# Performance work log

Measured on AMD Instinct MI355X. Metric: run time of the kernel, lower is better.

Reference implementation:

```python
import jax, jax.numpy as jnp
import numpy as np

B, S, D, H = 2, 2048, 1024, 16
DK = D // H
MAX_REL = 2047          # clip range for relative distances
REL_DIM = 64            # rel_embedding dim, summed over


def setup_inputs() -> dict:
    key = jax.random.key(0)
    ks = jax.random.split(key, 12)
    sc = 1.0 / np.sqrt(D)
    inp = {
        "q": jax.random.normal(ks[0], (B, S, D), jnp.float32),
        "k": jax.random.normal(ks[1], (B, S, D), jnp.float32),
        "v": jax.random.normal(ks[2], (B, S, D), jnp.float32),
        "Wq": jax.random.normal(ks[3], (D, D), jnp.float32) * sc,
        "bq": jnp.zeros((D,), jnp.float32),
        "Wk": jax.random.normal(ks[4], (D, D), jnp.float32) * sc,
        "bk": jnp.zeros((D,), jnp.float32),
        "Wv": jax.random.normal(ks[5], (D, D), jnp.float32) * sc,
        "bv": jnp.zeros((D,), jnp.float32),
        "Wo": jax.random.normal(ks[6], (D, D), jnp.float32) * sc,
        "bo": jnp.zeros((D,), jnp.float32),
        "rel_table": jax.random.normal(ks[7], (2 * MAX_REL + 1, REL_DIM), jnp.float32) * 0.02,
        "mask": jnp.tril(jnp.ones((1, 1, S, S), jnp.bool_)),  # causal
    }
    return inp


def reference(q, k, v, Wq, bq, Wk, bk, Wv, bv, Wo, bo, rel_table, mask):
    def split_heads(x):
        # [B,S,D] -> [B,H,S,DK]
        return x.reshape(B, -1, H, DK).transpose(0, 2, 1, 3)

    Q = split_heads(q @ Wq + bq)
    K = split_heads(k @ Wk + bk)
    V = split_heads(v @ Wv + bv)

    scores = jnp.einsum("bhqd,bhkd->bhqk", Q, K) / jnp.sqrt(jnp.float32(DK))

    # relative position bias: table[clip(j - i)] summed over rel dim -> [S,S]
    rel_idx = jnp.clip(jnp.arange(S)[None, :] - jnp.arange(S)[:, None],
                       -MAX_REL, MAX_REL) + MAX_REL
    rel_bias = rel_table[rel_idx].sum(-1)  # [S,S]
    scores = scores + rel_bias[None, None]

    scores = jnp.where(mask, scores, jnp.float32(-1e20))
    attn = jax.nn.softmax(scores, axis=-1)

    out = jnp.einsum("bhqk,bhkd->bhqd", attn, V)
    out = out.transpose(0, 2, 1, 3).reshape(B, -1, D)
    return out @ Wo + bo
```

## Files before the change

### kernel.cpp

```cpp
#include <hip/hip_runtime.h>

#define SEQ 2048
#define DIM 1024
#define NH 16
#define HD 64
#define NB 2

typedef __bf16 bf16x8 __attribute__((ext_vector_type(8)));
typedef float f32x4 __attribute__((ext_vector_type(4)));
typedef float f32x4v __attribute__((ext_vector_type(4)));
typedef float f32x4u __attribute__((ext_vector_type(4), aligned(4)));
typedef unsigned short us8 __attribute__((ext_vector_type(8)));
typedef unsigned short us4 __attribute__((ext_vector_type(4)));

#define LOG2E 1.44269504f

__device__ __forceinline__ unsigned short bfbits(float f) {
  __bf16 h = (__bf16)f;
  return __builtin_bit_cast(unsigned short, h);
}

__global__ __launch_bounds__(256) void wconv4_kernel(
    const float* __restrict__ W0, const float* __restrict__ W1,
    const float* __restrict__ W2, const float* __restrict__ W3,
    unsigned short* __restrict__ Wt, const float* __restrict__ rel_table,
    float* __restrict__ relsum) {
  int z = blockIdx.z;
  int tid = threadIdx.x;
  if (z == 4) {
    int ti = blockIdx.y * 16 + blockIdx.x;
    int i = ti * 256 + tid;
    if (i < 4095) {
      const f32x4v* row = reinterpret_cast<const f32x4v*>(rel_table + (size_t)i * 64);
      float s = 0.f;
      for (int d = 0; d < 16; ++d) {
        f32x4v v = row[d];
        s += v[0] + v[1] + v[2] + v[3];
      }
      relsum[i] = s * LOG2E;
    }
    return;
  }
  __shared__ unsigned short T[64][68];
  const float* W = (z == 0) ? W0 : (z == 1) ? W1 : (z == 2) ? W2 : W3;
  unsigned short* out = Wt + (size_t)z * 1024 * 1024;
  int r0 = blockIdx.y * 64;
  int c0 = blockIdx.x * 64;
  for (int it = 0; it < 4; ++it) {
    int s = tid + it * 256;
    int r = s >> 4;
    int c4 = (s & 15) * 4;
    f32x4v v = *reinterpret_cast<const f32x4v*>(W + (size_t)(r0 + r) * 1024 + c0 + c4);
    us4 o;
    o[0] = bfbits(v[0]); o[1] = bfbits(v[1]); o[2] = bfbits(v[2]); o[3] = bfbits(v[3]);
    *reinterpret_cast<us4*>(&T[r][c4]) = o;
  }
  __syncthreads();
  for (int it = 0; it < 2; ++it) {
    int s = tid + it * 256;
    int n = s >> 3;
    int k8 = (s & 7) * 8;
    us8 o;
    for (int e = 0; e < 8; ++e) o[e] = T[k8 + e][n];
    *reinterpret_cast<us8*>(out + (size_t)(c0 + n) * 1024 + r0 + k8) = o;
  }
}

__global__ __launch_bounds__(256) void gemm_qkv_kernel(
    const float* __restrict__ Aq, const float* __restrict__ Ak,
    const float* __restrict__ Av, const unsigned short* __restrict__ WTb,
    const float* __restrict__ bq, const float* __restrict__ bk,
    const float* __restrict__ bv, unsigned short* __restrict__ Qb,
    unsigned short* __restrict__ Kb, unsigned short* __restrict__ Vt,
    float qscale) {
  constexpr int N = 1024, K = 1024;
  int o = (blockIdx.x & 7) * 192 + (blockIdx.x >> 3);
  int row0 = (o / 48) * 128;
  int colz = o % 48;
  int z = colz >> 4;
  int col0 = (colz & 15) * 64;
  const float* A = (z == 0) ? Aq : (z == 1) ? Ak : Av;
  const unsigned short* WT = WTb + (size_t)z * N * K;
  const float* bias = (z == 0) ? bq : (z == 1) ? bk : bv;
  float oscale = (z == 0) ? qscale : 1.0f;

  int tid = threadIdx.x;
  int w = tid >> 6;
  int lane = tid & 63;
  int lg = lane >> 4;
  int li = lane & 15;
  int wr = (w >> 1) * 64;
  int wc = (w & 1) * 32;

  __shared__ unsigned short As[2][128][72];
  __shared__ unsigned short Ws[2][64][72];

  f32x4v af32[8];
  us8 wreg[2];

#define GLOAD(KS)                                                         \
  {                                                                       \
    int k0 = (KS) * 64;                                                   \
    for (int it = 0; it < 8; ++it) {                                      \
      int s = tid + it * 256;                                             \
      int r = s >> 4;                                                     \
      int cg = (s & 15) * 4;                                              \
      af32[it] = *reinterpret_cast<const f32x4v*>(                        \
          A + (size_t)(row0 + r) * K + k0 + cg);                          \
    }                                                                     \
    for (int it = 0; it < 2; ++it) {                                      \
      int s = tid + it * 256;                                             \
      int c = s >> 3;                                                     \
      int kg = (s & 7) * 8;                                               \
      wreg[it] = *reinterpret_cast<const us8*>(                           \
          WT + (size_t)(col0 + c) * K + k0 + kg);                         \
    }                                                                     \
  }

#define SWRITE(B)                                                         \
  {                                                                       \
    for (int it = 0; it < 8; ++it) {                                      \
      int s = tid + it * 256;                                             \
      int r = s >> 4;                                                     \
      int cg = (s & 15) * 4;                                              \
      us4 o2;                                                             \
      o2[0] = bfbits(af32[it][0]); o2[1] = bfbits(af32[it][1]);           \
      o2[2] = bfbits(af32[it][2]); o2[3] = bfbits(af32[it][3]);           \
      *reinterpret_cast<us4*>(&As[B][r][cg]) = o2;                        \
    }                                                                     \
    for (int it = 0; it < 2; ++it) {                                      \
      int s = tid + it * 256;                                             \
      int c = s >> 3;                                                     \
      int kg = (s & 7) * 8;                                               \
      *reinterpret_cast<us8*>(&Ws[B][c][kg]) = wreg[it];                  \
    }                                                                     \
  }

  f32x4 acc[4][2] = {};

  GLOAD(0);
  SWRITE(0);
  GLOAD(1);
  __syncthreads();

  for (int ks = 0; ks < 16; ++ks) {
    if (ks < 15) SWRITE((ks + 1) & 1);
    if (ks < 14) GLOAD(ks + 2);
    int B = ks & 1;
    for (int kk = 0; kk < 2; ++kk) {
      bf16x8 af[4], bfr[2];
      for (int m = 0; m < 4; ++m)
        af[m] = *reinterpret_cast<const bf16x8*>(&As[B][wr + m * 16 + li][kk * 32 + lg * 8]);
      for (int n = 0; n < 2; ++n)
        bfr[n] = *reinterpret_cast<const bf16x8*>(&Ws[B][wc + n * 16 + li][kk * 32 + lg * 8]);
      for (int m = 0; m < 4; ++m)
        for (int n = 0; n < 2; ++n)
          acc[m][n] = __builtin_amdgcn_mfma_f32_16x16x32_bf16(af[m], bfr[n], acc[m][n], 0, 0, 0);
    }
    __syncthreads();
  }

  for (int m = 0; m < 4; ++m)
    for (int n = 0; n < 2; ++n) {
      int row = row0 + wr + m * 16 + lg * 4;
      int col = col0 + wc + n * 16 + li;
      float v4[4];
      for (int r = 0; r < 4; ++r) v4[r] = (acc[m][n][r] + bias[col]) * oscale;
      if (z == 2) {
        int bb = row >> 11, seq = row & 2047;
        int hh = col >> 6, dk = col & 63;
        us4 o4;
        o4[0] = bfbits(v4[0]); o4[1] = bfbits(v4[1]);
        o4[2] = bfbits(v4[2]); o4[3] = bfbits(v4[3]);
        *reinterpret_cast<us4*>(
            Vt + ((size_t)(bb * NH + hh) * HD + dk) * SEQ + seq) = o4;
      } else {
        unsigned short* Cp = (z == 0) ? Qb : Kb;
        for (int r = 0; r < 4; ++r)
          Cp[(size_t)(row + r) * N + col] = bfbits(v4[r]);
      }
    }
#undef GLOAD
#undef SWRITE
}

__global__ __launch_bounds__(256) void gemm_out_kernel(
    const unsigned short* __restrict__ A, const unsigned short* __restrict__ WT,
    const float* __restrict__ bias, float* __restrict__ Cp) {
  constexpr int N = 1024, K = 1024;
  int o = ((blockIdx.x & 7) << 6) | (blockIdx.x >> 3);
  int col0 = (o & 15) * 64;
  int row0 = (o >> 4) * 128;
  int tid = threadIdx.x;
  int w = tid >> 6;
  int lane = tid & 63;
  int lg = lane >> 4;
  int li = lane & 15;
  int wr = (w >> 1) * 64;
  int wc = (w & 1) * 32;

  __shared__ unsigned short As[2][128][72];
  __shared__ unsigned short Ws[2][64][72];

  us8 ab16[4];
  us8 wreg[2];

#define GLOAD(KS)                                                         \
  {                                                                       \
    int k0 = (KS) * 64;                                                   \
    for (int it = 0; it < 4; ++it) {                                      \
      int s = tid + it * 256;                                             \
      int r = s >> 3;                                                     \
      int cg = (s & 7) * 8;                                               \
      ab16[it] = *reinterpret_cast<const us8*>(                           \
          A + (size_t)(row0 + r) * K + k0 + cg);                          \
    }                                                                     \
    for (int it = 0; it < 2; ++it) {                                      \
      int s = tid + it * 256;                                             \
      int c = s >> 3;                                                     \
      int kg = (s & 7) * 8;                                               \
      wreg[it] = *reinterpret_cast<const us8*>(                           \
          WT + (size_t)(col0 + c) * K + k0 + kg);                         \
    }                                                                     \
  }

#define SWRITE(B)                                                         \
  {                                                                       \
    for (int it = 0; it < 4; ++it) {                                      \
      int s = tid + it * 256;                                             \
      int r = s >> 3;                                                     \
      int cg = (s & 7) * 8;                                               \
      *reinterpret_cast<us8*>(&As[B][r][cg]) = ab16[it];                  \
    }                                                                     \
    for (int it = 0; it < 2; ++it) {                                      \
      int s = tid + it * 256;                                             \
      int c = s >> 3;                                                     \
      int kg = (s & 7) * 8;                                               \
      *reinterpret_cast<us8*>(&Ws[B][c][kg]) = wreg[it];                  \
    }                                                                     \
  }

  f32x4 acc[4][2] = {};

  GLOAD(0);
  SWRITE(0);
  GLOAD(1);
  __syncthreads();

  for (int ks = 0; ks < 16; ++ks) {
    if (ks < 15) SWRITE((ks + 1) & 1);
    if (ks < 14) GLOAD(ks + 2);
    int B = ks & 1;
    for (int kk = 0; kk < 2; ++kk) {
      bf16x8 af[4], bfr[2];
      for (int m = 0; m < 4; ++m)
        af[m] = *reinterpret_cast<const bf16x8*>(&As[B][wr + m * 16 + li][kk * 32 + lg * 8]);
      for (int n = 0; n < 2; ++n)
        bfr[n] = *reinterpret_cast<const bf16x8*>(&Ws[B][wc + n * 16 + li][kk * 32 + lg * 8]);
      for (int m = 0; m < 4; ++m)
        for (int n = 0; n < 2; ++n)
          acc[m][n] = __builtin_amdgcn_mfma_f32_16x16x32_bf16(af[m], bfr[n], acc[m][n], 0, 0, 0);
    }
    __syncthreads();
  }

  for (int m = 0; m < 4; ++m)
    for (int n = 0; n < 2; ++n)
      for (int r = 0; r < 4; ++r) {
        int row = row0 + wr + m * 16 + lg * 4 + r;
        int col = col0 + wc + n * 16 + li;
        Cp[(size_t)row * N + col] = acc[m][n][r] + bias[col];
      }
#undef GLOAD
#undef SWRITE
}

__global__ __launch_bounds__(256) void attn_kernel(
    const unsigned short* __restrict__ Qb, const unsigned short* __restrict__ Kb,
    const unsigned short* __restrict__ Vt, const float* __restrict__ relsum,
    unsigned short* __restrict__ Ob) {
  int o = ((blockIdx.x & 7) << 6) | (blockIdx.x >> 3);
  int p = o & 15;
  int h = (o >> 4) & 15;
  int b = o >> 8;

  int tid = threadIdx.x;
  int w = tid >> 6;
  int lane = tid & 63;
  int lg = lane >> 4;
  int li = lane & 15;

  __shared__ unsigned short Ks[128][72];
  __shared__ unsigned short VtF[2][64 * 72];
  __shared__ __bf16 Ps[4][16][136];
  __shared__ float rel_lds[2176];

  for (int it = 0; it < 3; ++it) {
    int slot = tid + it * 256;
    if (slot < 544)
      *reinterpret_cast<f32x4v*>(&rel_lds[slot * 4]) =
          *reinterpret_cast<const f32x4v*>(&relsum[slot * 4]);
  }

  int key0 = tid >> 3;
  int cg0 = (tid & 7) * 8;
  int dk0 = tid >> 3;
  int k8 = (tid & 7) * 8;
  const unsigned short* kptr = Kb + ((size_t)(b * SEQ + key0)) * DIM + h * HD + cg0;
  const unsigned short* vtp = Vt + ((size_t)(b * NH + h) * HD + dk0) * SEQ + k8;

  unsigned vidx0 = ((unsigned)(dk0 * 72 + k8)) ^ ((((unsigned)dk0 >> 3) & 7u) << 3);
  unsigned vidx1 = ((unsigned)((dk0 + 32) * 72 + k8)) ^
                   ((((unsigned)(dk0 + 32) >> 3) & 7u) << 3);

  us8 krg[4], vrg[4];

#define LOAD_REGS(TT)                                                     \
  {                                                                       \
    size_t koff = (size_t)(TT) * 128 * DIM;                               \
    krg[0] = *reinterpret_cast<const us8*>(kptr + koff);                  \
    krg[1] = *reinterpret_cast<const us8*>(kptr + koff + 32 * DIM);       \
    krg[2] = *reinterpret_cast<const us8*>(kptr + koff + 64 * DIM);       \
    krg[3] = *reinterpret_cast<const us8*>(kptr + koff + 96 * DIM);       \
    vrg[0] = *reinterpret_cast<const us8*>(vtp + (TT) * 128);             \
    vrg[1] = *reinterpret_cast<const us8*>(vtp + 32 * SEQ + (TT) * 128);  \
    vrg[2] = *reinterpret_cast<const us8*>(vtp + (TT) * 128 + 64);        \
    vrg[3] = *reinterpret_cast<const us8*>(vtp + 32 * SEQ + (TT) * 128 + 64); \
  }

#define WRITE_TILE()                                                     \
  {                                                                      \
    *reinterpret_cast<us8*>(&Ks[key0][cg0]) = krg[0];                    \
    *reinterpret_cast<us8*>(&Ks[key0 + 32][cg0]) = krg[1];               \
    *reinterpret_cast<us8*>(&Ks[key0 + 64][cg0]) = krg[2];               \
    *reinterpret_cast<us8*>(&Ks[key0 + 96][cg0]) = krg[3];               \
    *reinterpret_cast<us8*>(&VtF[0][vidx0]) = vrg[0];                    \
    *reinterpret_cast<us8*>(&VtF[0][vidx1]) = vrg[1];                    \
    *reinterpret_cast<us8*>(&VtF[1][vidx0]) = vrg[2];                    \
    *reinterpret_cast<us8*>(&VtF[1][vidx1]) = vrg[3];                    \
  }

  LOAD_REGS(0);

  for (int ph = 0; ph < 2; ++ph) {
    int qt = ph ? p : (31 - p);
    int nkv = (qt + 2) >> 1;

    int qrow = qt * 64 + w * 16 + li;
    const unsigned short* qb = Qb + ((size_t)(b * SEQ + qrow)) * DIM + h * HD;
    bf16x8 qa0 = *reinterpret_cast<const bf16x8*>(qb + lg * 8);
    bf16x8 qa1 = *reinterpret_cast<const bf16x8*>(qb + 32 + lg * 8);

    f32x4 o_acc[4] = {};
    float m_row[4], l_row[4];
    for (int r = 0; r < 4; ++r) { m_row[r] = -3e38f; l_row[r] = 0.f; }
    int i0 = qt * 64 + w * 16 + lg * 4;

    for (int t = 0; t < nkv; ++t) {
      __syncthreads();
      WRITE_TILE();
      __syncthreads();

      if (!(ph == 1 && t == nkv - 1)) {
        int nextT = (t + 1 < nkv) ? (t + 1) : 0;
        LOAD_REGS(nextT);
      }

      f32x4 s_acc[8] = {};
      __builtin_amdgcn_s_setprio(1);
      for (int kk = 0; kk < 2; ++kk) {
        bf16x8 qa = kk ? qa1 : qa0;
        for (int n = 0; n < 8; ++n) {
          bf16x8 kb = *reinterpret_cast<const bf16x8*>(&Ks[n * 16 + li][kk * 32 + lg * 8]);
          s_acc[n] = __builtin_amdgcn_mfma_f32_16x16x32_bf16(qa, kb, s_acc[n], 0, 0, 0);
        }
      }
      __builtin_amdgcn_s_setprio(0);

      float tmax[4] = {-3e38f, -3e38f, -3e38f, -3e38f};
      int Cbase = t * 128 - (qt * 64 + w * 16 + lg * 4) + li + 2047;
      if (t == nkv - 1) {
        for (int n = 0; n < 8; ++n) {
          int Cn = Cbase + n * 16;
          f32x4u rel4 = *reinterpret_cast<const f32x4u*>(&rel_lds[Cn - 3]);
          for (int r = 0; r < 4; ++r) {
            float sv = s_acc[n][r] + rel4[3 - r];
            sv = (Cn - r > 2047) ? -1e30f : sv;
            s_acc[n][r] = sv;
            tmax[r] = fmaxf(tmax[r], sv);
          }
        }
      } else {
        for (int n = 0; n < 8; ++n) {
          int Cn = Cbase + n * 16;
          f32x4u rel4 = *reinterpret_cast<const f32x4u*>(&rel_lds[Cn - 3]);
          for (int r = 0; r < 4; ++r) {
            float sv = s_acc[n][r] + rel4[3 - r];
            s_acc[n][r] = sv;
            tmax[r] = fmaxf(tmax[r], sv);
          }
        }
      }

      bool okl = true;
      for (int r = 0; r < 4; ++r) okl &= (tmax[r] <= m_row[r] + 8.f);
      if (!__all(okl)) {
        for (int msk = 1; msk < 16; msk <<= 1)
          for (int r = 0; r < 4; ++r)
            tmax[r] = fmaxf(tmax[r], __shfl_xor(tmax[r], msk));
        for (int r = 0; r < 4; ++r) {
          float mn = fmaxf(m_row[r], tmax[r]);
          float al = exp2f(m_row[r] - mn);
          m_row[r] = mn;
          l_row[r] *= al;
          o_acc[0][r] *= al; o_acc[1][r] *= al;
          o_acc[2][r] *= al; o_acc[3][r] *= al;
        }
      }

      for (int n = 0; n < 8; ++n)
        for (int r = 0; r < 4; ++r) {
          float e = exp2f(s_acc[n][r] - m_row[r]);
          s_acc[n][r] = e;
          l_row[r] += e;
        }

      for (int n = 0; n < 8; ++n)
        for (int r = 0; r < 4; ++r)
          Ps[w][lg * 4 + r][n * 16 + li] = (__bf16)s_acc[n][r];
      asm volatile("s_waitcnt lgkmcnt(0)" ::: "memory");
      __builtin_amdgcn_sched_barrier(0);

      __builtin_amdgcn_s_setprio(1);
      for (int kstep = 0; kstep < 4; ++kstep) {
        int half = kstep >> 1;
        int kk = kstep & 1;
        bf16x8 pa = *reinterpret_cast<const bf16x8*>(&Ps[w][li][kstep * 32 + lg * 8]);
        for (int n = 0; n < 4; ++n) {
          int dk = n * 16 + li;
          unsigned idx = ((unsigned)(dk * 72 + kk * 32 + lg * 8)) ^
                         ((((unsigned)dk >> 3) & 7u) << 3);
          bf16x8 vb = *reinterpret_cast<const bf16x8*>(&VtF[half][idx]);
          o_acc[n] = __builtin_amdgcn_mfma_f32_16x16x32_bf16(pa, vb, o_acc[n], 0, 0, 0);
        }
      }
      __builtin_amdgcn_s_setprio(0);
    }

    for (int msk = 1; msk < 16; msk <<= 1)
      for (int r = 0; r < 4; ++r) l_row[r] += __shfl_xor(l_row[r], msk);
    float inv_l[4];
    for (int r = 0; r < 4; ++r) inv_l[r] = 1.f / l_row[r];
    for (int n = 0; n < 4; ++n)
      for (int r = 0; r < 4; ++r) {
        int row = i0 + r;
        int dk = n * 16 + li;
        Ob[((size_t)(b * SEQ + row)) * DIM + h * HD + dk] =
            bfbits(o_acc[n][r] * inv_l[r]);
      }
  }
#undef LOAD_REGS
#undef WRITE_TILE
}

extern "C" void kernel_launch(void* const* d_in, const int* in_sizes, int n_in,
                              void* d_out, int out_size, void* d_ws, size_t ws_size,
                              hipStream_t stream) {
  const float* q = (const float*)d_in[0];
  const float* k = (const float*)d_in[1];
  const float* v = (const float*)d_in[2];
  const float* Wq = (const float*)d_in[3];
  const float* bq = (const float*)d_in[4];
  const float* Wk = (const float*)d_in[5];
  const float* bk = (const float*)d_in[6];
  const float* Wv = (const float*)d_in[7];
  const float* bv = (const float*)d_in[8];
  const float* Wo = (const float*)d_in[9];
  const float* bo = (const float*)d_in[10];
  const float* rel = (const float*)d_in[11];

  char* ws = (char*)d_ws;
  const size_t MATB = (size_t)NB * SEQ * DIM * sizeof(unsigned short);
  const size_t WTE = (size_t)DIM * DIM;
  unsigned short* Qb = (unsigned short*)(ws);
  unsigned short* Kb = (unsigned short*)(ws + MATB);
  unsigned short* Vt = (unsigned short*)(ws + 2 * MATB);
  unsigned short* Ob = (unsigned short*)(ws + 3 * MATB);
  float* relsum = (float*)(ws + 4 * MATB);
  unsigned short* WT = (unsigned short*)(ws + 4 * MATB + 65536);

  wconv4_kernel<<<dim3(16, 16, 5), 256, 0, stream>>>(Wq, Wk, Wv, Wo, WT, rel, relsum);

  const float qscale = 0.125f * LOG2E;
  gemm_qkv_kernel<<<dim3(1536), 256, 0, stream>>>(q, k, v, WT, bq, bk, bv,
                                                  Qb, Kb, Vt, qscale);

  attn_kernel<<<dim3(512), 256, 0, stream>>>(Qb, Kb, Vt, relsum, Ob);

  gemm_out_kernel<<<dim3(512), 256, 0, stream>>>(Ob, WT + 3 * WTE, bo, (float*)d_out);
}
```

Baseline: 144.4 us.

## Pre-convert QKV activations to bf16 in setup kernel before projection GEMM

Extends the weight-conversion kernel with extra z-slices that convert q, k, v from fp32 to bf16. The bf16 copies go into scratch space borrowed from the output buffer and the attention-output buffer. The QKV GEMM then loads half as many bytes per A tile and skips the per-iteration conversion. Block-to-tile mapping also changes so each group of 512 consecutive tiles shares one projection, which affects L2 reuse. The cost is an extra pass over the activations (fp32 read plus bf16 write) before the GEMM.

New measurement: 136.9 us. 1.05x faster.

```diff
diff --git a/kernel.cpp b/kernel.cpp
--- a/kernel.cpp
+++ b/kernel.cpp
@@ -24,7 +24,10 @@
     const float* __restrict__ W0, const float* __restrict__ W1,
     const float* __restrict__ W2, const float* __restrict__ W3,
     unsigned short* __restrict__ Wt, const float* __restrict__ rel_table,
-    float* __restrict__ relsum) {
+    float* __restrict__ relsum, const float* __restrict__ Aq,
+    const float* __restrict__ Ak, const float* __restrict__ Av,
+    unsigned short* __restrict__ Bq, unsigned short* __restrict__ Bk,
+    unsigned short* __restrict__ Bv) {
   int z = blockIdx.z;
   int tid = threadIdx.x;
   if (z == 4) {
@@ -38,6 +41,22 @@
         s += v[0] + v[1] + v[2] + v[3];
       }
       relsum[i] = s * LOG2E;
+    }
+    return;
+  }
+  if (z >= 5) {
+    const float* src = (z == 5) ? Aq : (z == 6) ? Ak : Av;
+    unsigned short* dst = (z == 5) ? Bq : (z == 6) ? Bk : Bv;
+    int bid2 = blockIdx.y * 16 + blockIdx.x;
+    int c0 = bid2 * 256 + tid;
+    for (int j = 0; j < 8; ++j) {
+      size_t e = ((size_t)(c0 + j * 65536)) * 8;
+      f32x4v v0 = *reinterpret_cast<const f32x4v*>(src + e);
+      f32x4v v1 = *reinterpret_cast<const f32x4v*>(src + e + 4);
+      us8 o;
+      o[0] = bfbits(v0[0]); o[1] = bfbits(v0[1]); o[2] = bfbits(v0[2]); o[3] = bfbits(v0[3]);
+      o[4] = bfbits(v1[0]); o[5] = bfbits(v1[1]); o[6] = bfbits(v1[2]); o[7] = bfbits(v1[3]);
+      *reinterpret_cast<us8*>(dst + e) = o;
     }
     return;
   }
@@ -67,19 +86,19 @@
 }
 
 __global__ __launch_bounds__(256) void gemm_qkv_kernel(
-    const float* __restrict__ Aq, const float* __restrict__ Ak,
-    const float* __restrict__ Av, const unsigned short* __restrict__ WTb,
+    const unsigned short* __restrict__ Aq, const unsigned short* __restrict__ Ak,
+    const unsigned short* __restrict__ Av, const unsigned short* __restrict__ WTb,
     const float* __restrict__ bq, const float* __restrict__ bk,
     const float* __restrict__ bv, unsigned short* __restrict__ Qb,
     unsigned short* __restrict__ Kb, unsigned short* __restrict__ Vt,
     float qscale) {
   constexpr int N = 1024, K = 1024;
   int o = (blockIdx.x & 7) * 192 + (blockIdx.x >> 3);
-  int row0 = (o / 48) * 128;
-  int colz = o % 48;
-  int z = colz >> 4;
-  int col0 = (colz & 15) * 64;
-  const float* A = (z == 0) ? Aq : (z == 1) ? Ak : Av;
+  int z = o >> 9;
+  int r2 = o & 511;
+  int row0 = (r2 >> 4) * 128;
+  int col0 = (r2 & 15) * 64;
+  const unsigned short* A = (z == 0) ? Aq : (z == 1) ? Ak : Av;
   const unsigned short* WT = WTb + (size_t)z * N * K;
   const float* bias = (z == 0) ? bq : (z == 1) ? bk : bv;
   float oscale = (z == 0) ? qscale : 1.0f;
@@ -95,17 +114,17 @@
   __shared__ unsigned short As[2][128][72];
   __shared__ unsigned short Ws[2][64][72];
 
-  f32x4v af32[8];
+  us8 ab16[4];
   us8 wreg[2];
 
 #define GLOAD(KS)                                                         \
   {                                                                       \
     int k0 = (KS) * 64;                                                   \
-    for (int it = 0; it < 8; ++it) {                                      \
-      int s = tid + it * 256;                                             \
-      int r = s >> 4;                                                     \
-      int cg = (s & 15) * 4;                                              \
-      af32[it] = *reinterpret_cast<const f32x4v*>(                        \
+    for (int it = 0; it < 4; ++it) {                                      \
+      int s = tid + it * 256;                                             \
+      int r = s >> 3;                                                     \
+      int cg = (s & 7) * 8;                                               \
+      ab16[it] = *reinterpret_cast<const us8*>(                           \
           A + (size_t)(row0 + r) * K + k0 + cg);                          \
     }                                                                     \
     for (int it = 0; it < 2; ++it) {                                      \
@@ -119,14 +138,11 @@
 
 #define SWRITE(B)                                                         \
   {                                                                       \
-    for (int it = 0; it < 8; ++it) {                                      \
-      int s = tid + it * 256;                                             \
-      int r = s >> 4;                                                     \
-      int cg = (s & 15) * 4;                                              \
-      us4 o2;                                                             \
-      o2[0] = bfbits(af32[it][0]); o2[1] = bfbits(af32[it][1]);           \
-      o2[2] = bfbits(af32[it][2]); o2[3] = bfbits(af32[it][3]);           \
-      *reinterpret_cast<us4*>(&As[B][r][cg]) = o2;                        \
+    for (int it = 0; it < 4; ++it) {                                      \
+      int s = tid + it * 256;                                             \
+      int r = s >> 3;                                                     \
+      int cg = (s & 7) * 8;                                               \
+      *reinterpret_cast<us8*>(&As[B][r][cg]) = ab16[it];                  \
     }                                                                     \
     for (int it = 0; it < 2; ++it) {                                      \
       int s = tid + it * 256;                                             \
@@ -489,10 +505,15 @@
   float* relsum = (float*)(ws + 4 * MATB);
   unsigned short* WT = (unsigned short*)(ws + 4 * MATB + 65536);
 
-  wconv4_kernel<<<dim3(16, 16, 5), 256, 0, stream>>>(Wq, Wk, Wv, Wo, WT, rel, relsum);
+  unsigned short* Abq = (unsigned short*)d_out;
+  unsigned short* Abk = (unsigned short*)d_out + (size_t)NB * SEQ * DIM;
+  unsigned short* Abv = Ob;
+
+  wconv4_kernel<<<dim3(16, 16, 8), 256, 0, stream>>>(
+      Wq, Wk, Wv, Wo, WT, rel, relsum, q, k, v, Abq, Abk, Abv);
 
   const float qscale = 0.125f * LOG2E;
-  gemm_qkv_kernel<<<dim3(1536), 256, 0, stream>>>(q, k, v, WT, bq, bk, bv,
+  gemm_qkv_kernel<<<dim3(1536), 256, 0, stream>>>(Abq, Abk, Abv, WT, bq, bk, bv,
                                                   Qb, Kb, Vt, qscale);
 
   attn_kernel<<<dim3(512), 256, 0, stream>>>(Qb, Kb, Vt, relsum, Ob);
```
